# Optimization experiments

Hardware: AMD Instinct MI355X
Metric: run time of the kernel (lower is better)

The kernel has to match this reference:

```python
import jax, jax.numpy as jnp
import numpy as np

N = 100000   # num_nodes
E = 1600000  # num_edges (avg degree 16)
D = 64       # embed_channels
C = 16       # num_classes
EPSILON = 0.1  # AntiSymmetricConv step size (PyG default)
GAMMA = 0.1    # AntiSymmetricConv diffusion strength (PyG default)


def setup_inputs() -> dict:
    key = jax.random.key(0)
    ks = jax.random.split(key, 9)
    s = 1.0 / np.sqrt(D)
    return {
        "edge_index": jax.random.randint(ks[0], (2, E), 0, N, dtype=jnp.int32),
        "embed_w": jax.random.normal(ks[1], (N, D), dtype=jnp.float32) * 0.1,
        "W_rel": jax.random.normal(ks[2], (D, D), dtype=jnp.float32) * s,   # GraphConv lin_rel weight
        "b_rel": jax.random.normal(ks[3], (D,), dtype=jnp.float32) * s,     # GraphConv lin_rel bias
        "W_root": jax.random.normal(ks[4], (D, D), dtype=jnp.float32) * s,  # GraphConv lin_root weight (no bias)
        "W_anti": jax.random.normal(ks[5], (D, D), dtype=jnp.float32) * s,  # AntiSymmetricConv W
        "b_anti": jax.random.normal(ks[6], (D,), dtype=jnp.float32) * s,    # AntiSymmetricConv bias
        "W_lin": jax.random.normal(ks[7], (C, D), dtype=jnp.float32) * s,   # lin2 weight
        "b_lin": jax.random.normal(ks[8], (C,), dtype=jnp.float32) * s,     # lin2 bias
    }


def reference(edge_index, embed_w, W_rel, b_rel, W_root, W_anti, b_anti, W_lin, b_lin):
    x = embed_w  # [N, D] node features = embedding table
    src, dst = edge_index[0], edge_index[1]
    # phi = GraphConv with 'add' aggregation: lin_rel(sum_j x_j) + lin_root(x)
    agg = jax.ops.segment_sum(x[src], dst, num_segments=N)  # [N, D] sparse gather+scatter-add
    h = agg @ W_rel.T + b_rel + x @ W_root.T
    # antisymmetric weight: W - W^T - gamma * I
    aW = W_anti - W_anti.T - GAMMA * jnp.eye(D, dtype=x.dtype)
    h = x @ aW.T + h + b_anti
    h = jnp.tanh(h)                       # default act of AntiSymmetricConv
    x = x + EPSILON * h                   # single iteration (num_iters=1 default)
    # dropout p=0.0 -> identity
    out = jax.nn.sigmoid(x @ W_lin.T + b_lin)  # [N, C]
    return out
```

## Files before the change

### kernel.cpp

```cpp
#include <hip/hip_runtime.h>
#include <hip/hip_fp16.h>

#define DD 64
#define CC 16
#define EPSILON 0.1f
#define GAMMA 0.1f
#define BSH 6
#define BSZ 64
#define CAP 1280
#define MAXBK 2048
#define PAD 65
#define CSH 10
#define MAXNC 128
#define CAPC 17408
#define L1CHUNK 4096
#define L1THR 512
#define NSLICE 8

__global__ __launch_bounds__(256) void prep_all(
        const float* __restrict__ x, __half2* __restrict__ xh2,
        int* __restrict__ gcntc, int* __restrict__ gcnt,
        const float* __restrict__ Wrel, const float* __restrict__ Wroot,
        const float* __restrict__ Wanti, const float* __restrict__ brel,
        const float* __restrict__ banti,
        float* __restrict__ B_g, float* __restrict__ bc, int N) {
    const int t = threadIdx.x, b = blockIdx.x, G = gridDim.x;
    for (int i = b * 256 + t; i < MAXNC + MAXBK; i += G * 256) {
        if (i < MAXNC) gcntc[i] = 0;
        else gcnt[i - MAXNC] = 0;
    }
    const float2* x2 = (const float2*)x;
    const int M = N * (DD / 2);
    for (int i = b * 256 + t; i < M; i += G * 256)
        xh2[i] = __float22half2_rn(x2[i]);
    if (b == 0) {
        for (int idx = t; idx < 128 * 64; idx += 256) {
            int k = idx >> 6, d = idx & 63;
            float v;
            if (k < 64) {
                v = Wrel[d * 64 + k];
            } else {
                int j = k - 64;
                v = Wroot[d * 64 + j] + Wanti[d * 64 + j] - Wanti[j * 64 + d];
                if (d == j) v -= GAMMA;
            }
            B_g[idx] = v;
        }
        if (t < 64) bc[t] = brel[t] + banti[t];
    }
}

__global__ __launch_bounds__(L1THR) void bin_coarse(const int* __restrict__ ei,
                                                    int* __restrict__ gcntc,
                                                    unsigned* __restrict__ binned_c,
                                                    int E) {
    __shared__ int hist[MAXNC];
    __shared__ int hbase[MAXNC];
    const int t = threadIdx.x;
    if (t < MAXNC) hist[t] = 0;
    __syncthreads();
    const int e0 = blockIdx.x * L1CHUNK;
    int dsts[L1CHUNK / L1THR];
#pragma unroll
    for (int i = 0; i < L1CHUNK / L1THR; ++i) {
        int e = e0 + t + L1THR * i;
        dsts[i] = (e < E) ? ei[E + e] : -1;
        if (dsts[i] >= 0) atomicAdd(&hist[dsts[i] >> CSH], 1);
    }
    __syncthreads();
    if (t < MAXNC) {
        hbase[t] = hist[t] ? atomicAdd(&gcntc[t], hist[t]) : 0;
        hist[t] = 0;
    }
    __syncthreads();
#pragma unroll
    for (int i = 0; i < L1CHUNK / L1THR; ++i) {
        if (dsts[i] >= 0) {
            int e = e0 + t + L1THR * i;
            int src = ei[e];
            int c = dsts[i] >> CSH;
            int pos = hbase[c] + atomicAdd(&hist[c], 1);
            if (pos < CAPC)
                binned_c[(size_t)c * CAPC + pos] =
                    (unsigned)src | ((unsigned)(dsts[i] & ((1 << CSH) - 1)) << 17);
        }
    }
}

__global__ __launch_bounds__(256) void bin_fine(const int* __restrict__ gcntc,
                                                const unsigned* __restrict__ binned_c,
                                                int* __restrict__ gcnt,
                                                unsigned* __restrict__ binned) {
    __shared__ int hist[16];
    __shared__ int hbase[16];
    const int t = threadIdx.x;
    const int c = blockIdx.x >> 3, s = blockIdx.x & (NSLICE - 1);
    int cnt = gcntc[c];
    if (cnt > CAPC) cnt = CAPC;
    const int per = (cnt + NSLICE - 1) / NSLICE;
    const int i0 = s * per;
    int i1 = i0 + per;
    if (i1 > cnt) i1 = cnt;
    if (t < 16) hist[t] = 0;
    __syncthreads();
    const unsigned* bcp = binned_c + (size_t)c * CAPC;
    unsigned ent[9];
#pragma unroll
    for (int j = 0; j < 9; ++j) {
        int i = i0 + t + j * 256;
        ent[j] = (i < i1) ? bcp[i] : 0xFFFFFFFFu;
        if (ent[j] != 0xFFFFFFFFu) atomicAdd(&hist[ent[j] >> (17 + BSH)], 1);
    }
    __syncthreads();
    if (t < 16) {
        hbase[t] = hist[t] ? atomicAdd(&gcnt[c * 16 + t], hist[t]) : 0;
        hist[t] = 0;
    }
    __syncthreads();
#pragma unroll
    for (int j = 0; j < 9; ++j) {
        if (ent[j] != 0xFFFFFFFFu) {
            unsigned dstc = ent[j] >> 17;
            int f = dstc >> BSH;
            int pos = hbase[f] + atomicAdd(&hist[f], 1);
            if (pos < CAP)
                binned[(size_t)(c * 16 + f) * CAP + pos] =
                    (ent[j] & 0x1FFFF) | ((dstc & (BSZ - 1)) << 17);
        }
    }
}

__global__ __launch_bounds__(512, 8) void mega(
        const float* __restrict__ x, const __half* __restrict__ x_h,
        const int* __restrict__ gcnt, const unsigned* __restrict__ binned,
        const float* __restrict__ B_g, const float* __restrict__ bc,
        const float* __restrict__ Wlin, const float* __restrict__ blin,
        float* __restrict__ out, int N) {
    __shared__ float R0[BSZ * PAD];
    __shared__ float wl_sh[CC * PAD];
    __shared__ int csr[CAP];
    __shared__ int deg[BSZ], offs[BSZ], cur[BSZ];

    const int t = threadIdx.x;
    const int b = blockIdx.x;
    const int nb0 = b << BSH;
    int cnt = gcnt[b];
    if (cnt > CAP) cnt = CAP;
    const unsigned* bl = binned + (size_t)b * CAP;

#pragma unroll
    for (int i = 0; i < 2; ++i) {
        int idx = t + 512 * i;
        wl_sh[(idx >> 6) * PAD + (idx & 63)] = Wlin[idx];
    }
    if (t < BSZ) deg[t] = 0;
    __syncthreads();
    for (int i = t; i < cnt; i += 512) atomicAdd(&deg[bl[i] >> 17], 1);
    __syncthreads();
    if (t < BSZ) offs[t] = deg[t];
    __syncthreads();
    for (int off = 1; off < BSZ; off <<= 1) {
        int v = 0;
        if (t < BSZ && t >= off) v = offs[t - off];
        __syncthreads();
        if (t < BSZ) offs[t] += v;
        __syncthreads();
    }
    if (t < BSZ) {
        int excl = offs[t] - deg[t];
        offs[t] = excl;
        cur[t] = excl;
    }
    __syncthreads();
    for (int i = t; i < cnt; i += 512) {
        unsigned en = bl[i];
        int pos = atomicAdd(&cur[en >> 17], 1);
        csr[pos] = (int)(en & 0x1FFFF);
    }
    __syncthreads();

    {
        const int g = t >> 3, q = t & 7;
        const float4* xh4 = (const float4*)x_h;
        const int i0 = offs[g], dc = deg[g];
        __half2 z = __floats2half2_rn(0.f, 0.f);
        __half2 A0[4] = {z, z, z, z}, A1[4] = {z, z, z, z};
        __half2 A2[4] = {z, z, z, z}, A3[4] = {z, z, z, z};
        int i = 0;
        for (; i + 4 <= dc; i += 4) {
            int s0 = csr[i0 + i], s1 = csr[i0 + i + 1];
            int s2 = csr[i0 + i + 2], s3 = csr[i0 + i + 3];
            float4 v0 = xh4[s0 * 8 + q];
            float4 v1 = xh4[s1 * 8 + q];
            float4 v2 = xh4[s2 * 8 + q];
            float4 v3 = xh4[s3 * 8 + q];
            const __half2* h0 = (const __half2*)&v0;
            const __half2* h1 = (const __half2*)&v1;
            const __half2* h2 = (const __half2*)&v2;
            const __half2* h3 = (const __half2*)&v3;
#pragma unroll
            for (int r = 0; r < 4; ++r) {
                A0[r] = __hadd2(A0[r], h0[r]);
                A1[r] = __hadd2(A1[r], h1[r]);
                A2[r] = __hadd2(A2[r], h2[r]);
                A3[r] = __hadd2(A3[r], h3[r]);
            }
        }
        for (; i < dc; ++i) {
            int s0 = csr[i0 + i];
            float4 v0 = xh4[s0 * 8 + q];
            const __half2* h0 = (const __half2*)&v0;
#pragma unroll
            for (int r = 0; r < 4; ++r) A0[r] = __hadd2(A0[r], h0[r]);
        }
        float* row = &R0[g * PAD + 8 * q];
#pragma unroll
        for (int r = 0; r < 4; ++r) {
            float2 f0 = __half22float2(A0[r]);
            float2 f1 = __half22float2(A1[r]);
            float2 f2 = __half22float2(A2[r]);
            float2 f3 = __half22float2(A3[r]);
            row[2 * r] = (f0.x + f1.x) + (f2.x + f3.x);
            row[2 * r + 1] = (f0.y + f1.y) + (f2.y + f3.y);
        }
    }
    __syncthreads();

    const int nl = t & 63;
    const int dgw = __builtin_amdgcn_readfirstlane(t >> 6);
    float acc[8];
#pragma unroll
    for (int j = 0; j < 8; ++j) acc[j] = 0.f;
#pragma unroll 8
    for (int k = 0; k < DD; ++k) {
        float a = R0[nl * PAD + k];
        const float* Bk = &B_g[k * DD + dgw * 8];
#pragma unroll
        for (int j = 0; j < 8; ++j) acc[j] = fmaf(a, Bk[j], acc[j]);
    }
    __syncthreads();

    {
        int nn = N - nb0;
        if (nn > BSZ) nn = BSZ;
        const float4* x4 = (const float4*)x;
        for (int idx = t; idx < nn * 16; idx += 512) {
            float4 v = x4[nb0 * 16 + idx];
            float* row = &R0[(idx >> 4) * PAD + (idx & 15) * 4];
            row[0] = v.x; row[1] = v.y; row[2] = v.z; row[3] = v.w;
        }
    }
    __syncthreads();

#pragma unroll 8
    for (int k = 0; k < DD; ++k) {
        float a = R0[nl * PAD + k];
        const float* Bk = &B_g[(DD + k) * DD + dgw * 8];
#pragma unroll
        for (int j = 0; j < 8; ++j) acc[j] = fmaf(a, Bk[j], acc[j]);
    }

#pragma unroll
    for (int j = 0; j < 8; ++j) {
        int d = dgw * 8 + j;
        float h = acc[j] + bc[d];
        float e2 = __expf(2.0f * h);
        float th = 1.0f - 2.0f / (e2 + 1.0f);
        acc[j] = R0[nl * PAD + d] + EPSILON * th;
    }
    __syncthreads();
#pragma unroll
    for (int j = 0; j < 8; ++j) R0[nl * PAD + dgw * 8 + j] = acc[j];
    __syncthreads();

    {
        const int g = t >> 3, q = t & 7;
        const int n = nb0 + g;
        if (n < N) {
            float p0 = blin[2 * q], p1 = blin[2 * q + 1];
#pragma unroll 8
            for (int d = 0; d < DD; ++d) {
                float xv = R0[g * PAD + d];
                p0 = fmaf(xv, wl_sh[(2 * q) * PAD + d], p0);
                p1 = fmaf(xv, wl_sh[(2 * q + 1) * PAD + d], p1);
            }
            float2 o;
            o.x = 1.0f / (1.0f + __expf(-p0));
            o.y = 1.0f / (1.0f + __expf(-p1));
            *(float2*)(out + (size_t)n * CC + 2 * q) = o;
        }
    }
}

extern "C" void kernel_launch(void* const* d_in, const int* in_sizes, int n_in,
                              void* d_out, int out_size, void* d_ws, size_t ws_size,
                              hipStream_t stream) {
    const int*   ei    = (const int*)d_in[0];
    const float* x     = (const float*)d_in[1];
    const float* Wrel  = (const float*)d_in[2];
    const float* brel  = (const float*)d_in[3];
    const float* Wroot = (const float*)d_in[4];
    const float* Wanti = (const float*)d_in[5];
    const float* banti = (const float*)d_in[6];
    const float* Wlin  = (const float*)d_in[7];
    const float* blin  = (const float*)d_in[8];
    float* out = (float*)d_out;

    const int E = in_sizes[0] / 2;
    const int N = in_sizes[1] / DD;
    const int NBK = (N + BSZ - 1) >> BSH;
    const int NC  = (N + (1 << CSH) - 1) >> CSH;

    __half* x_h = (__half*)d_ws;
    unsigned* binned_c = (unsigned*)(x_h + (size_t)N * DD);
    unsigned* binned = binned_c + (size_t)MAXNC * CAPC;
    int*   gcntc = (int*)(binned + (size_t)MAXBK * CAP);
    int*   gcnt  = gcntc + MAXNC;
    float* B_g   = (float*)(gcnt + MAXBK);
    float* bc    = B_g + 128 * 64;

    prep_all<<<512, 256, 0, stream>>>(x, (__half2*)x_h, gcntc, gcnt, Wrel,
                                      Wroot, Wanti, brel, banti, B_g, bc, N);
    bin_coarse<<<(E + L1CHUNK - 1) / L1CHUNK, L1THR, 0, stream>>>(ei, gcntc, binned_c, E);
    bin_fine<<<NC * NSLICE, 256, 0, stream>>>(gcntc, binned_c, gcnt, binned);
    mega<<<NBK, 512, 0, stream>>>(x, x_h, gcnt, binned, B_g, bc, Wlin, blin, out, N);
}
```

Measured before the change: 184.1 us.

## Drop fine binning kernel, filter coarse buckets in mega, sort-then-coalesce coarse binning

Removes the bin_fine pass. Each mega block now scans its whole coarse bucket and uses ballot-based compaction to pick out the edges for its 64-node fine bin. bin_coarse now does a local counting sort in shared memory so its global writes are contiguous per bucket, and it uses a smaller chunk. The root-term reload of x now reads the fp16 copy instead of fp32, which cuts traffic but lowers the precision of the x term. In exchange, every coarse bucket is read 16 times by different blocks, and mega uses more shared memory.

```diff
diff --git a/kernel.cpp b/kernel.cpp
--- a/kernel.cpp
+++ b/kernel.cpp
@@ -8,32 +8,27 @@
 #define BSH 6
 #define BSZ 64
 #define CAP 1280
-#define MAXBK 2048
 #define PAD 65
 #define CSH 10
 #define MAXNC 128
 #define CAPC 17408
-#define L1CHUNK 4096
+#define L1CHUNK 2048
 #define L1THR 512
-#define NSLICE 8
 
 __global__ __launch_bounds__(256) void prep_all(
         const float* __restrict__ x, __half2* __restrict__ xh2,
-        int* __restrict__ gcntc, int* __restrict__ gcnt,
+        int* __restrict__ gcntc,
         const float* __restrict__ Wrel, const float* __restrict__ Wroot,
         const float* __restrict__ Wanti, const float* __restrict__ brel,
         const float* __restrict__ banti,
         float* __restrict__ B_g, float* __restrict__ bc, int N) {
     const int t = threadIdx.x, b = blockIdx.x, G = gridDim.x;
-    for (int i = b * 256 + t; i < MAXNC + MAXBK; i += G * 256) {
-        if (i < MAXNC) gcntc[i] = 0;
-        else gcnt[i - MAXNC] = 0;
-    }
+    if (b == 0 && t < MAXNC) gcntc[t] = 0;
     const float2* x2 = (const float2*)x;
     const int M = N * (DD / 2);
     for (int i = b * 256 + t; i < M; i += G * 256)
         xh2[i] = __float22half2_rn(x2[i]);
-    if (b == 0) {
+    if (b == G - 1) {
         for (int idx = t; idx < 128 * 64; idx += 256) {
             int k = idx >> 6, d = idx & 63;
             float v;
@@ -54,99 +49,76 @@
                                                     int* __restrict__ gcntc,
                                                     unsigned* __restrict__ binned_c,
                                                     int E) {
-    __shared__ int hist[MAXNC];
-    __shared__ int hbase[MAXNC];
+    __shared__ unsigned sorted[L1CHUNK];
+    __shared__ unsigned char bkt[L1CHUNK];
+    __shared__ int hist[MAXNC], base[MAXNC], cur[MAXNC], gbase[MAXNC];
     const int t = threadIdx.x;
     if (t < MAXNC) hist[t] = 0;
     __syncthreads();
     const int e0 = blockIdx.x * L1CHUNK;
-    int dsts[L1CHUNK / L1THR];
+    unsigned ent[L1CHUNK / L1THR];
+    int cbk[L1CHUNK / L1THR];
 #pragma unroll
     for (int i = 0; i < L1CHUNK / L1THR; ++i) {
         int e = e0 + t + L1THR * i;
-        dsts[i] = (e < E) ? ei[E + e] : -1;
-        if (dsts[i] >= 0) atomicAdd(&hist[dsts[i] >> CSH], 1);
-    }
-    __syncthreads();
-    if (t < MAXNC) {
-        hbase[t] = hist[t] ? atomicAdd(&gcntc[t], hist[t]) : 0;
-        hist[t] = 0;
-    }
-    __syncthreads();
-#pragma unroll
-    for (int i = 0; i < L1CHUNK / L1THR; ++i) {
-        if (dsts[i] >= 0) {
-            int e = e0 + t + L1THR * i;
-            int src = ei[e];
-            int c = dsts[i] >> CSH;
-            int pos = hbase[c] + atomicAdd(&hist[c], 1);
-            if (pos < CAPC)
-                binned_c[(size_t)c * CAPC + pos] =
-                    (unsigned)src | ((unsigned)(dsts[i] & ((1 << CSH) - 1)) << 17);
-        }
+        cbk[i] = -1;
+        if (e < E) {
+            int src = ei[e], dst = ei[E + e];
+            cbk[i] = dst >> CSH;
+            ent[i] = (unsigned)src | ((unsigned)(dst & ((1 << CSH) - 1)) << 17);
+            atomicAdd(&hist[cbk[i]], 1);
+        }
+    }
+    __syncthreads();
+    if (t < MAXNC) cur[t] = hist[t];
+    __syncthreads();
+    for (int off = 1; off < MAXNC; off <<= 1) {
+        int v = 0;
+        if (t < MAXNC && t >= off) v = cur[t - off];
+        __syncthreads();
+        if (t < MAXNC) cur[t] += v;
+        __syncthreads();
+    }
+    if (t < MAXNC) { base[t] = cur[t] - hist[t]; cur[t] = base[t]; }
+    __syncthreads();
+#pragma unroll
+    for (int i = 0; i < L1CHUNK / L1THR; ++i)
+        if (cbk[i] >= 0) {
+            int pos = atomicAdd(&cur[cbk[i]], 1);
+            sorted[pos] = ent[i];
+            bkt[pos] = (unsigned char)cbk[i];
+        }
+    __syncthreads();
+    if (t < MAXNC) gbase[t] = hist[t] ? atomicAdd(&gcntc[t], hist[t]) : 0;
+    __syncthreads();
+    int m = E - e0;
+    if (m > L1CHUNK) m = L1CHUNK;
+    for (int j = t; j < m; j += L1THR) {
+        int cb = bkt[j];
+        int gp = gbase[cb] + (j - base[cb]);
+        if (gp < CAPC) binned_c[(size_t)cb * CAPC + gp] = sorted[j];
     }
 }
 
-__global__ __launch_bounds__(256) void bin_fine(const int* __restrict__ gcntc,
-                                                const unsigned* __restrict__ binned_c,
-                                                int* __restrict__ gcnt,
-                                                unsigned* __restrict__ binned) {
-    __shared__ int hist[16];
-    __shared__ int hbase[16];
-    const int t = threadIdx.x;
-    const int c = blockIdx.x >> 3, s = blockIdx.x & (NSLICE - 1);
-    int cnt = gcntc[c];
-    if (cnt > CAPC) cnt = CAPC;
-    const int per = (cnt + NSLICE - 1) / NSLICE;
-    const int i0 = s * per;
-    int i1 = i0 + per;
-    if (i1 > cnt) i1 = cnt;
-    if (t < 16) hist[t] = 0;
-    __syncthreads();
-    const unsigned* bcp = binned_c + (size_t)c * CAPC;
-    unsigned ent[9];
-#pragma unroll
-    for (int j = 0; j < 9; ++j) {
-        int i = i0 + t + j * 256;
-        ent[j] = (i < i1) ? bcp[i] : 0xFFFFFFFFu;
-        if (ent[j] != 0xFFFFFFFFu) atomicAdd(&hist[ent[j] >> (17 + BSH)], 1);
-    }
-    __syncthreads();
-    if (t < 16) {
-        hbase[t] = hist[t] ? atomicAdd(&gcnt[c * 16 + t], hist[t]) : 0;
-        hist[t] = 0;
-    }
-    __syncthreads();
-#pragma unroll
-    for (int j = 0; j < 9; ++j) {
-        if (ent[j] != 0xFFFFFFFFu) {
-            unsigned dstc = ent[j] >> 17;
-            int f = dstc >> BSH;
-            int pos = hbase[f] + atomicAdd(&hist[f], 1);
-            if (pos < CAP)
-                binned[(size_t)(c * 16 + f) * CAP + pos] =
-                    (ent[j] & 0x1FFFF) | ((dstc & (BSZ - 1)) << 17);
-        }
-    }
-}
-
 __global__ __launch_bounds__(512, 8) void mega(
-        const float* __restrict__ x, const __half* __restrict__ x_h,
-        const int* __restrict__ gcnt, const unsigned* __restrict__ binned,
+        const __half* __restrict__ x_h,
+        const int* __restrict__ gcntc, const unsigned* __restrict__ binned_c,
         const float* __restrict__ B_g, const float* __restrict__ bc,
         const float* __restrict__ Wlin, const float* __restrict__ blin,
         float* __restrict__ out, int N) {
     __shared__ float R0[BSZ * PAD];
     __shared__ float wl_sh[CC * PAD];
+    __shared__ int tmp[CAP];
     __shared__ int csr[CAP];
     __shared__ int deg[BSZ], offs[BSZ], cur[BSZ];
+    __shared__ int mcount;
 
     const int t = threadIdx.x;
-    const int b = blockIdx.x;
-    const int nb0 = b << BSH;
-    int cnt = gcnt[b];
-    if (cnt > CAP) cnt = CAP;
-    const unsigned* bl = binned + (size_t)b * CAP;
+    const int c = blockIdx.x >> 4, f = blockIdx.x & 15;
+    const int nb0 = (c << CSH) + (f << BSH);
+    int cnt_c = gcntc[c];
+    if (cnt_c > CAPC) cnt_c = CAPC;
+    const unsigned* bcl = binned_c + (size_t)c * CAPC;
 
 #pragma unroll
     for (int i = 0; i < 2; ++i) {
@@ -154,8 +126,33 @@
         wl_sh[(idx >> 6) * PAD + (idx & 63)] = Wlin[idx];
     }
     if (t < BSZ) deg[t] = 0;
-    __syncthreads();
-    for (int i = t; i < cnt; i += 512) atomicAdd(&deg[bl[i] >> 17], 1);
+    if (t == 0) mcount = 0;
+    __syncthreads();
+
+    {
+        const int lane = t & 63;
+        for (int i = t; i < cnt_c; i += 512) {
+            unsigned en = bcl[i];
+            bool pred = ((en >> (17 + BSH)) & 15) == (unsigned)f;
+            unsigned long long msk = __ballot(pred);
+            if (msk) {
+                int lead = __ffsll((long long)msk) - 1;
+                int bse = 0;
+                if (lane == lead) bse = atomicAdd(&mcount, __popcll(msk));
+                bse = __shfl(bse, lead);
+                if (pred) {
+                    int p = bse + __popcll(msk & ((1ull << lane) - 1ull));
+                    if (p < CAP)
+                        tmp[p] = (int)((en & 0x1FFFF) | (((en >> 17) & 63) << 17));
+                }
+            }
+        }
+    }
+    __syncthreads();
+    int cnt = mcount;
+    if (cnt > CAP) cnt = CAP;
+
+    for (int i = t; i < cnt; i += 512) atomicAdd(&deg[tmp[i] >> 17], 1);
     __syncthreads();
     if (t < BSZ) offs[t] = deg[t];
     __syncthreads();
@@ -173,9 +170,9 @@
     }
     __syncthreads();
     for (int i = t; i < cnt; i += 512) {
-        unsigned en = bl[i];
+        int en = tmp[i];
         int pos = atomicAdd(&cur[en >> 17], 1);
-        csr[pos] = (int)(en & 0x1FFFF);
+        csr[pos] = en & 0x1FFFF;
     }
     __syncthreads();
 
@@ -243,11 +240,17 @@
     {
         int nn = N - nb0;
         if (nn > BSZ) nn = BSZ;
-        const float4* x4 = (const float4*)x;
-        for (int idx = t; idx < nn * 16; idx += 512) {
-            float4 v = x4[nb0 * 16 + idx];
-            float* row = &R0[(idx >> 4) * PAD + (idx & 15) * 4];
-            row[0] = v.x; row[1] = v.y; row[2] = v.z; row[3] = v.w;
+        const float4* xh4 = (const float4*)x_h;
+        for (int idx = t; idx < nn * 8; idx += 512) {
+            float4 v = xh4[(size_t)nb0 * 8 + idx];
+            const __half2* h = (const __half2*)&v;
+            float* row = &R0[(idx >> 3) * PAD + (idx & 7) * 8];
+#pragma unroll
+            for (int r = 0; r < 4; ++r) {
+                float2 fv = __half22float2(h[r]);
+                row[2 * r] = fv.x;
+                row[2 * r + 1] = fv.y;
+            }
         }
     }
     __syncthreads();
@@ -308,20 +311,16 @@
 
     const int E = in_sizes[0] / 2;
     const int N = in_sizes[1] / DD;
-    const int NBK = (N + BSZ - 1) >> BSH;
-    const int NC  = (N + (1 << CSH) - 1) >> CSH;
+    const int NC = (N + (1 << CSH) - 1) >> CSH;
 
     __half* x_h = (__half*)d_ws;
     unsigned* binned_c = (unsigned*)(x_h + (size_t)N * DD);
-    unsigned* binned = binned_c + (size_t)MAXNC * CAPC;
-    int*   gcntc = (int*)(binned + (size_t)MAXBK * CAP);
-    int*   gcnt  = gcntc + MAXNC;
-    float* B_g   = (float*)(gcnt + MAXBK);
+    int*   gcntc = (int*)(binned_c + (size_t)MAXNC * CAPC);
+    float* B_g   = (float*)(gcntc + MAXNC);
     float* bc    = B_g + 128 * 64;
 
-    prep_all<<<512, 256, 0, stream>>>(x, (__half2*)x_h, gcntc, gcnt, Wrel,
+    prep_all<<<512, 256, 0, stream>>>(x, (__half2*)x_h, gcntc, Wrel,
                                       Wroot, Wanti, brel, banti, B_g, bc, N);
     bin_coarse<<<(E + L1CHUNK - 1) / L1CHUNK, L1THR, 0, stream>>>(ei, gcntc, binned_c, E);
-    bin_fine<<<NC * NSLICE, 256, 0, stream>>>(gcntc, binned_c, gcnt, binned);
-    mega<<<NBK, 512, 0, stream>>>(x, x_h, gcnt, binned, B_g, bc, Wlin, blin, out, N);
+    mega<<<NC * 16, 512, 0, stream>>>(x_h, gcntc, binned_c, B_g, bc, Wlin, blin, out, N);
 }
```

After: 199.7 us. 1.08x slower.
